# Performance work log

Hardware: AMD Instinct MI355X
Metric: run time of the kernel (lower is better)

## Reference

```python
import jax, jax.numpy as jnp
import numpy as np

NEG_BIG = -1e38

def setup_inputs() -> dict:
    key = jax.random.key(0)
    kq, kk, kv, kwq, kwk = jax.random.split(key, 5)
    B, S, d_model, d_k, d_v = 4, 4096, 256, 64, 64
    return {
        "q": jax.random.normal(kq, (B, S, d_model), dtype=jnp.float32),
        "k": jax.random.normal(kk, (B, S, d_model), dtype=jnp.float32),
        "v": jax.random.normal(kv, (B, S, d_v), dtype=jnp.float32),
        "w_q": jax.random.normal(kwq, (d_k, d_model), dtype=jnp.float32) * 0.01,
        "w_k": jax.random.normal(kwk, (d_k, d_model), dtype=jnp.float32) * 0.01,
    }

def reference(q, k, v, w_q, w_k):
    d_k = w_q.shape[0]
    temperature = jnp.asarray(np.power(d_k, 0.5), dtype=q.dtype)
    # relu-projected Q, K: [B,S,d_k]
    qp = jax.nn.relu(jnp.einsum("bsm,km->bsk", q, w_q))
    kp = jax.nn.relu(jnp.einsum("bsm,km->bsk", k, w_k))
    # scores [B,S,S]
    attn = jnp.einsum("bqd,bkd->bqk", qp, kp) / temperature
    # force column 0 to -1e38 (inline custom mask)
    attn = attn.at[:, :, 0].set(NEG_BIG)
    attn = jax.nn.softmax(attn, axis=2)
    # dropout is identity in eval / p=0
    out = jnp.einsum("bqk,bkd->bqd", attn, v)
    return out
```

## Files before the change

### kernel.cpp

```cpp
#include <hip/hip_runtime.h>

#define B_    4
#define S_    4096
#define DM    256
#define DK    64
#define NROWS (B_ * S_)
#define LOG2E 1.4426950408889634f
#define PACK_BIAS 0.0028151295f
#define NSPLIT 2
#define NJ     16

typedef __attribute__((ext_vector_type(8))) short bfrag;
typedef __attribute__((ext_vector_type(4))) float ffrag;

__device__ __forceinline__ unsigned bf16_rne_hi(float x) {
    unsigned u = __float_as_uint(x);
    return u + 0x7fffu + ((u >> 16) & 1u);
}
__device__ __forceinline__ unsigned short f2bf(float x) {
    return (unsigned short)(bf16_rne_hi(x) >> 16);
}
__device__ __forceinline__ unsigned pack_bf16x2(float lo, float hi) {
    return (bf16_rne_hi(hi) & 0xffff0000u) | (bf16_rne_hi(lo) >> 16);
}

__device__ __forceinline__ float fast_exp2(float x) {
#if __has_builtin(__builtin_amdgcn_exp2f)
    return __builtin_amdgcn_exp2f(x);
#else
    float r;
    asm("v_exp_f32 %0, %1\n\ts_nop 1" : "=v"(r) : "v"(x));
    return r;
#endif
}

__device__ __forceinline__ unsigned trunc_pack_bf16x2(float lo, float hi) {
    return __builtin_amdgcn_perm(__float_as_uint(hi), __float_as_uint(lo),
                                 0x07060302u);
}

__global__ __launch_bounds__(256) void fused_prep(
    const float* __restrict__ q, const float* __restrict__ k,
    const float* __restrict__ v, const float* __restrict__ wq,
    const float* __restrict__ wk, unsigned short* __restrict__ vT,
    unsigned short* __restrict__ qpb, unsigned short* __restrict__ kpb)
{
    __shared__ __align__(16) char smem[50688];
    const int blk  = blockIdx.x;
    const int lane = threadIdx.x & 63, w = threadIdx.x >> 6;

    if (blk < 256) {
        float (*tile)[65] = (float(*)[65])smem;
        const int b = blk >> 6, s0 = (blk & 63) * 64;
        const float4* src = (const float4*)(v + (size_t)(b * S_ + s0) * DK);
#pragma unroll
        for (int i = 0; i < 4; ++i) {
            const int idx4 = i * 256 + threadIdx.x;
            const int row = idx4 >> 4, c4 = idx4 & 15;
            const float4 vv = src[idx4];
            tile[row][c4 * 4 + 0] = vv.x;
            tile[row][c4 * 4 + 1] = vv.y;
            tile[row][c4 * 4 + 2] = vv.z;
            tile[row][c4 * 4 + 3] = vv.w;
        }
        __syncthreads();
        unsigned* dst = (unsigned*)(vT + (size_t)(b * 128 + (s0 >> 5)) * 64 * 32);
#pragma unroll
        for (int i = 0; i < 8; ++i) {
            const int u = i * 256 + threadIdx.x;
            const int t32 = u >> 10, rem = u & 1023;
            const int d = rem >> 4, c = rem & 15;
            dst[(t32 * 64 + d) * 16 + c] =
                pack_bf16x2(tile[t32 * 32 + c][d], tile[t32 * 32 + c + 16][d]);
        }
    } else {
        unsigned short* xlds = (unsigned short*)smem;
        unsigned short* wlds = (unsigned short*)(smem + 16896);
        const int pb = blk - 256;
        const int half = pb >> 9, rblk = pb & 511;
        const float* x;
        const float* wsrc;
        unsigned short* o;
        float scale;
        if (half == 0) { x = q; wsrc = wq; o = qpb; scale = 0.125f * LOG2E; }
        else           { x = k; wsrc = wk; o = kpb; scale = 1.0f; }

        const int rows0 = rblk * 32;
        const float4* xsrc = (const float4*)(x + (size_t)rows0 * DM);
#pragma unroll
        for (int i = 0; i < 8; ++i) {
            const int idx4 = i * 256 + threadIdx.x;
            const int row = idx4 >> 6, c4 = idx4 & 63;
            const float4 xv = xsrc[idx4];
            uint2 pk2;
            pk2.x = pack_bf16x2(xv.x, xv.y);
            pk2.y = pack_bf16x2(xv.z, xv.w);
            *(uint2*)&xlds[row * 264 + c4 * 4] = pk2;
        }
#pragma unroll
        for (int i = 0; i < 16; ++i) {
            const int idx4 = i * 256 + threadIdx.x;
            const int row = idx4 >> 6, c4 = idx4 & 63;
            const float4 wv = ((const float4*)wsrc)[idx4];
            uint2 pk2;
            pk2.x = pack_bf16x2(wv.x, wv.y);
            pk2.y = pack_bf16x2(wv.z, wv.w);
            *(uint2*)&wlds[row * 264 + c4 * 4] = pk2;
        }
        __syncthreads();

        const int m = lane & 15, quad = lane >> 4;

        ffrag acc[2];
        acc[0] = (ffrag)(0.0f);
        acc[1] = (ffrag)(0.0f);

#pragma unroll
        for (int kf = 0; kf < 8; ++kf) {
            const bfrag Bf = *(const bfrag*)&wlds[(w * 16 + m) * 264 + kf * 32 + quad * 8];
#pragma unroll
            for (int mt = 0; mt < 2; ++mt) {
                const bfrag A = *(const bfrag*)&xlds[(mt * 16 + m) * 264 + kf * 32 + quad * 8];
                acc[mt] = __builtin_amdgcn_mfma_f32_16x16x32_bf16(A, Bf, acc[mt], 0, 0, 0);
            }
        }
#pragma unroll
        for (int mt = 0; mt < 2; ++mt)
#pragma unroll
            for (int r = 0; r < 4; ++r)
                o[(rows0 + mt * 16 + quad * 4 + r) * DK + w * 16 + m] =
                    f2bf(fmaxf(acc[mt][r], 0.0f) * scale);
    }
}

__global__ __launch_bounds__(256) void attn_mfma(
    const unsigned short* __restrict__ qp, const unsigned short* __restrict__ kp,
    const unsigned short* __restrict__ vT, float* __restrict__ num_part,
    float* __restrict__ den_part)
{
    __shared__ __align__(16) char smem[20480];
    unsigned short* Plds = (unsigned short*)smem;
    float* red0 = (float*)smem;
    float* red1 = (float*)smem + 2560;

    const int lane = threadIdx.x & 63, w = threadIdx.x >> 6;
    const int m = lane & 15, quad = lane >> 4;
    const int sid = blockIdx.x & 7;
    const int b   = sid >> 1, gy = sid & 1;
    const int qgw = blockIdx.x >> 3;
    const int qbase = (b * 128 + qgw) * 32;
    const int kstart = (gy * 4 + w) * 512;

    bfrag qa[2][2];
#pragma unroll
    for (int mt = 0; mt < 2; ++mt)
#pragma unroll
        for (int kf = 0; kf < 2; ++kf)
            qa[mt][kf] = *(const bfrag*)&qp[(qbase + mt * 16 + m) * DK + kf * 32 + quad * 8];

    ffrag oacc[2][4];
    float dacc[2][4];
#pragma unroll
    for (int mt = 0; mt < 2; ++mt) {
#pragma unroll
        for (int dt = 0; dt < 4; ++dt) oacc[mt][dt] = (ffrag)(0.0f);
#pragma unroll
        for (int r = 0; r < 4; ++r) dacc[mt][r] = 0.0f;
    }

    const unsigned short* kptr = kp + ((size_t)b * S_ + kstart + m) * DK + quad * 8;
    const unsigned short* vptr = vT + ((size_t)(b * 128 + (kstart >> 5)) * 64 + m) * 32 + quad * 8;
    unsigned short* Pw = Plds + w * 1280;

    const ffrag cbias = (ffrag)(PACK_BIAS);

    bfrag kbuf[2][2][2], vbuf[2][4];
#pragma unroll
    for (int kt = 0; kt < 2; ++kt)
#pragma unroll
        for (int kf = 0; kf < 2; ++kf)
            kbuf[0][kt][kf] = *(const bfrag*)(kptr + kt * 1024 + kf * 32);
#pragma unroll
    for (int dt = 0; dt < 4; ++dt)
        vbuf[0][dt] = *(const bfrag*)(vptr + dt * 512);

    const unsigned short* knext = kptr + 2048;
    const unsigned short* vnext = vptr + 2048;

    bfrag pa0, pa1;

#pragma unroll 2
    for (int jj = 0; jj < NJ; ++jj) {
        const int p = jj & 1;

        if (jj < NJ - 1) {
#pragma unroll
            for (int kt = 0; kt < 2; ++kt)
#pragma unroll
                for (int kf = 0; kf < 2; ++kf)
                    kbuf[p ^ 1][kt][kf] = *(const bfrag*)(knext + kt * 1024 + kf * 32);
        }

        if (jj > 0) {
#pragma unroll
            for (int dt = 0; dt < 4; ++dt) {
                oacc[0][dt] = __builtin_amdgcn_mfma_f32_16x16x32_bf16(pa0, vbuf[p ^ 1][dt], oacc[0][dt], 0, 0, 0);
                oacc[1][dt] = __builtin_amdgcn_mfma_f32_16x16x32_bf16(pa1, vbuf[p ^ 1][dt], oacc[1][dt], 0, 0, 0);
            }
        }

        if (jj < NJ - 1) {
#pragma unroll
            for (int dt = 0; dt < 4; ++dt)
                vbuf[p ^ 1][dt] = *(const bfrag*)(vnext + dt * 512);
        }
        knext += 2048;
        vnext += 2048;

        ffrag s[2][2];
#pragma unroll
        for (int mt = 0; mt < 2; ++mt)
#pragma unroll
            for (int kt = 0; kt < 2; ++kt) {
                ffrag t = __builtin_amdgcn_mfma_f32_16x16x32_bf16(qa[mt][0], kbuf[p][kt][0], cbias, 0, 0, 0);
                s[mt][kt] = __builtin_amdgcn_mfma_f32_16x16x32_bf16(qa[mt][1], kbuf[p][kt][1], t, 0, 0, 0);
            }

        const bool mask0 = (jj == 0) && (kstart == 0) && (m == 0);
#pragma unroll
        for (int mt = 0; mt < 2; ++mt)
#pragma unroll
            for (int r = 0; r < 4; ++r) {
                float e0 = fast_exp2(s[mt][0][r]);
                float e1 = fast_exp2(s[mt][1][r]);
                if (mask0) e0 = 0.0f;
                dacc[mt][r] += e0 + e1;
                *(unsigned*)&Pw[(mt * 16 + quad * 4 + r) * 40 + m * 2] =
                    trunc_pack_bf16x2(e0, e1);
            }

        pa0 = *(const bfrag*)&Pw[(m) * 40 + quad * 8];
        pa1 = *(const bfrag*)&Pw[(16 + m) * 40 + quad * 8];
    }
#pragma unroll
    for (int dt = 0; dt < 4; ++dt) {
        oacc[0][dt] = __builtin_amdgcn_mfma_f32_16x16x32_bf16(pa0, vbuf[1][dt], oacc[0][dt], 0, 0, 0);
        oacc[1][dt] = __builtin_amdgcn_mfma_f32_16x16x32_bf16(pa1, vbuf[1][dt], oacc[1][dt], 0, 0, 0);
    }

#pragma unroll
    for (int mt = 0; mt < 2; ++mt)
#pragma unroll
        for (int r = 0; r < 4; ++r) {
            float d = dacc[mt][r];
            d += __shfl_xor(d, 1, 64);
            d += __shfl_xor(d, 2, 64);
            d += __shfl_xor(d, 4, 64);
            d += __shfl_xor(d, 8, 64);
            dacc[mt][r] = d;
        }

    __syncthreads();
    float* red[2] = { red0, red1 };
    if (w >= 2) {
#pragma unroll
        for (int mt = 0; mt < 2; ++mt) {
#pragma unroll
            for (int dt = 0; dt < 4; ++dt)
#pragma unroll
                for (int r = 0; r < 4; ++r)
                    red[w - 2][((mt * 4 + dt) * 4 + r) * 64 + lane] = oacc[mt][dt][r];
#pragma unroll
            for (int r = 0; r < 4; ++r)
                red[w - 2][2048 + (mt * 4 + r) * 64 + lane] = dacc[mt][r];
        }
    }
    __syncthreads();
    if (w < 2) {
#pragma unroll
        for (int mt = 0; mt < 2; ++mt) {
#pragma unroll
            for (int dt = 0; dt < 4; ++dt)
#pragma unroll
                for (int r = 0; r < 4; ++r)
                    oacc[mt][dt][r] += red[w][((mt * 4 + dt) * 4 + r) * 64 + lane];
#pragma unroll
            for (int r = 0; r < 4; ++r)
                dacc[mt][r] += red[w][2048 + (mt * 4 + r) * 64 + lane];
        }
    }
    __syncthreads();
    if (w == 1) {
#pragma unroll
        for (int mt = 0; mt < 2; ++mt) {
#pragma unroll
            for (int dt = 0; dt < 4; ++dt)
#pragma unroll
                for (int r = 0; r < 4; ++r)
                    red0[((mt * 4 + dt) * 4 + r) * 64 + lane] = oacc[mt][dt][r];
#pragma unroll
            for (int r = 0; r < 4; ++r)
                red0[2048 + (mt * 4 + r) * 64 + lane] = dacc[mt][r];
        }
    }
    __syncthreads();
    if (w == 0) {
#pragma unroll
        for (int mt = 0; mt < 2; ++mt) {
#pragma unroll
            for (int dt = 0; dt < 4; ++dt)
#pragma unroll
                for (int r = 0; r < 4; ++r) {
                    const float nv = oacc[mt][dt][r] + red0[((mt * 4 + dt) * 4 + r) * 64 + lane];
                    num_part[(size_t)gy * NROWS * DK +
                             (qbase + mt * 16 + quad * 4 + r) * DK + dt * 16 + m] = nv;
                }
#pragma unroll
            for (int r = 0; r < 4; ++r) {
                const float dv = dacc[mt][r] + red0[2048 + (mt * 4 + r) * 64 + lane];
                if (m == 0)
                    den_part[gy * NROWS + qbase + mt * 16 + quad * 4 + r] = dv;
            }
        }
    }
}

__global__ __launch_bounds__(256) void finalize_kernel(
    const float* __restrict__ num_part, const float* __restrict__ den_part,
    float* __restrict__ out)
{
    const int i4 = blockIdx.x * 256 + threadIdx.x;
    const int row = i4 >> 4;
    const float4 a = ((const float4*)num_part)[i4];
    const float4 c = ((const float4*)(num_part + (size_t)NROWS * DK))[i4];
    const float inv = 1.0f / (den_part[row] + den_part[NROWS + row]);
    float4 o;
    o.x = (a.x + c.x) * inv;
    o.y = (a.y + c.y) * inv;
    o.z = (a.z + c.z) * inv;
    o.w = (a.w + c.w) * inv;
    ((float4*)out)[i4] = o;
}

extern "C" void kernel_launch(void* const* d_in, const int* in_sizes, int n_in,
                              void* d_out, int out_size, void* d_ws, size_t ws_size,
                              hipStream_t stream)
{
    const float* q  = (const float*)d_in[0];
    const float* k  = (const float*)d_in[1];
    const float* v  = (const float*)d_in[2];
    const float* wq = (const float*)d_in[3];
    const float* wk = (const float*)d_in[4];
    float* out = (float*)d_out;

    char* p = (char*)d_ws;
    unsigned short* qpb = (unsigned short*)p;   p += (size_t)NROWS * DK * 2;
    unsigned short* kpb = (unsigned short*)p;   p += (size_t)NROWS * DK * 2;
    unsigned short* vT  = (unsigned short*)p;   p += (size_t)B_ * DK * S_ * 2;
    float* num_part     = (float*)p;            p += (size_t)NSPLIT * NROWS * DK * 4;
    float* den_part     = (float*)p;

    fused_prep<<<1280, 256, 0, stream>>>(q, k, v, wq, wk, vT, qpb, kpb);
    attn_mfma<<<1024, 256, 0, stream>>>(qpb, kpb, vT, num_part, den_part);
    finalize_kernel<<<NROWS * DK / 4 / 256, 256, 0, stream>>>(num_part, den_part, out);
}
```

Measured before the change: 139.5 us.

## Fuse prep, attention and finalize into one persistent kernel with grid barrier

Merges the three launches into a single 512-block kernel. Each block first does its share of the V transpose and Q/K projection, then waits on an atomic-counter grid barrier before running attention. The key split across blocks is removed, so each block now covers all keys with 4 waves of 1024 keys each and writes normalized output directly, dropping the partial numerator/denominator buffers and the finalize pass. The cost is a spin barrier that only works if all 512 blocks are resident at once, a memset launch to reset the counter, and half the grid parallelism in the attention phase with a longer per-wave loop.

Result: slower. 190.4 us (+36.5%).

```diff
diff --git a/kernel.cpp b/kernel.cpp
--- a/kernel.cpp
+++ b/kernel.cpp
@@ -7,8 +7,8 @@
 #define NROWS (B_ * S_)
 #define LOG2E 1.4426950408889634f
 #define PACK_BIAS 0.0028151295f
-#define NSPLIT 2
-#define NJ     16
+#define NJ 32
+#define GRID_BLKS 512
 
 typedef __attribute__((ext_vector_type(8))) short bfrag;
 typedef __attribute__((ext_vector_type(4))) float ffrag;
@@ -23,7 +23,6 @@
 __device__ __forceinline__ unsigned pack_bf16x2(float lo, float hi) {
     return (bf16_rne_hi(hi) & 0xffff0000u) | (bf16_rne_hi(lo) >> 16);
 }
-
 __device__ __forceinline__ float fast_exp2(float x) {
 #if __has_builtin(__builtin_amdgcn_exp2f)
     return __builtin_amdgcn_exp2f(x);
@@ -33,28 +32,29 @@
     return r;
 #endif
 }
-
 __device__ __forceinline__ unsigned trunc_pack_bf16x2(float lo, float hi) {
     return __builtin_amdgcn_perm(__float_as_uint(hi), __float_as_uint(lo),
                                  0x07060302u);
 }
 
-__global__ __launch_bounds__(256) void fused_prep(
+__global__ __launch_bounds__(256) void mega_kernel(
     const float* __restrict__ q, const float* __restrict__ k,
     const float* __restrict__ v, const float* __restrict__ wq,
-    const float* __restrict__ wk, unsigned short* __restrict__ vT,
-    unsigned short* __restrict__ qpb, unsigned short* __restrict__ kpb)
+    const float* __restrict__ wk, unsigned short* __restrict__ qpb,
+    unsigned short* __restrict__ kpb, unsigned short* __restrict__ vT,
+    unsigned* __restrict__ barrier_ctr, float* __restrict__ out)
 {
-    __shared__ __align__(16) char smem[50688];
-    const int blk  = blockIdx.x;
+    __shared__ __align__(16) char smem[20480];
     const int lane = threadIdx.x & 63, w = threadIdx.x >> 6;
-
-    if (blk < 256) {
+    const int m = lane & 15, quad = lane >> 4;
+    const int bp = blockIdx.x;
+
+    {
         float (*tile)[65] = (float(*)[65])smem;
-        const int b = blk >> 6, s0 = (blk & 63) * 64;
-        const float4* src = (const float4*)(v + (size_t)(b * S_ + s0) * DK);
-#pragma unroll
-        for (int i = 0; i < 4; ++i) {
+        const int b = bp >> 7, tt = bp & 127;
+        const float4* src = (const float4*)(v + ((size_t)b * S_ + tt * 32) * DK);
+#pragma unroll
+        for (int i = 0; i < 2; ++i) {
             const int idx4 = i * 256 + threadIdx.x;
             const int row = idx4 >> 4, c4 = idx4 & 15;
             const float4 vv = src[idx4];
@@ -64,99 +64,96 @@
             tile[row][c4 * 4 + 3] = vv.w;
         }
         __syncthreads();
-        unsigned* dst = (unsigned*)(vT + (size_t)(b * 128 + (s0 >> 5)) * 64 * 32);
-#pragma unroll
-        for (int i = 0; i < 8; ++i) {
+        unsigned* dst = (unsigned*)(vT + (size_t)bp * 2048);
+#pragma unroll
+        for (int i = 0; i < 4; ++i) {
             const int u = i * 256 + threadIdx.x;
-            const int t32 = u >> 10, rem = u & 1023;
-            const int d = rem >> 4, c = rem & 15;
-            dst[(t32 * 64 + d) * 16 + c] =
-                pack_bf16x2(tile[t32 * 32 + c][d], tile[t32 * 32 + c + 16][d]);
-        }
-    } else {
-        unsigned short* xlds = (unsigned short*)smem;
-        unsigned short* wlds = (unsigned short*)(smem + 16896);
-        const int pb = blk - 256;
-        const int half = pb >> 9, rblk = pb & 511;
-        const float* x;
-        const float* wsrc;
-        unsigned short* o;
-        float scale;
-        if (half == 0) { x = q; wsrc = wq; o = qpb; scale = 0.125f * LOG2E; }
-        else           { x = k; wsrc = wk; o = kpb; scale = 1.0f; }
-
-        const int rows0 = rblk * 32;
-        const float4* xsrc = (const float4*)(x + (size_t)rows0 * DM);
-#pragma unroll
-        for (int i = 0; i < 8; ++i) {
-            const int idx4 = i * 256 + threadIdx.x;
-            const int row = idx4 >> 6, c4 = idx4 & 63;
-            const float4 xv = xsrc[idx4];
-            uint2 pk2;
-            pk2.x = pack_bf16x2(xv.x, xv.y);
-            pk2.y = pack_bf16x2(xv.z, xv.w);
-            *(uint2*)&xlds[row * 264 + c4 * 4] = pk2;
-        }
-#pragma unroll
-        for (int i = 0; i < 16; ++i) {
-            const int idx4 = i * 256 + threadIdx.x;
-            const int row = idx4 >> 6, c4 = idx4 & 63;
-            const float4 wv = ((const float4*)wsrc)[idx4];
-            uint2 pk2;
-            pk2.x = pack_bf16x2(wv.x, wv.y);
-            pk2.y = pack_bf16x2(wv.z, wv.w);
-            *(uint2*)&wlds[row * 264 + c4 * 4] = pk2;
-        }
-        __syncthreads();
-
-        const int m = lane & 15, quad = lane >> 4;
-
-        ffrag acc[2];
-        acc[0] = (ffrag)(0.0f);
-        acc[1] = (ffrag)(0.0f);
-
+            const int d = u >> 4, c = u & 15;
+            dst[d * 16 + c] = pack_bf16x2(tile[c][d], tile[c + 16][d]);
+        }
+    }
+
+    {
+        const int half = bp >> 8, rblk = bp & 255;
+        const float* x = half ? k : q;
+        const float* wsrc = half ? wk : wq;
+        unsigned short* o = half ? kpb : qpb;
+        const float scale = half ? 1.0f : 0.125f * LOG2E;
+        const int rows0 = rblk * 64;
+
+        bfrag xa[8];
+        const float4* xrow = (const float4*)(x + (size_t)(rows0 + w * 16 + m) * DM);
 #pragma unroll
         for (int kf = 0; kf < 8; ++kf) {
-            const bfrag Bf = *(const bfrag*)&wlds[(w * 16 + m) * 264 + kf * 32 + quad * 8];
-#pragma unroll
-            for (int mt = 0; mt < 2; ++mt) {
-                const bfrag A = *(const bfrag*)&xlds[(mt * 16 + m) * 264 + kf * 32 + quad * 8];
-                acc[mt] = __builtin_amdgcn_mfma_f32_16x16x32_bf16(A, Bf, acc[mt], 0, 0, 0);
-            }
-        }
-#pragma unroll
-        for (int mt = 0; mt < 2; ++mt)
-#pragma unroll
-            for (int r = 0; r < 4; ++r)
-                o[(rows0 + mt * 16 + quad * 4 + r) * DK + w * 16 + m] =
-                    f2bf(fmaxf(acc[mt][r], 0.0f) * scale);
-    }
-}
-
-__global__ __launch_bounds__(256) void attn_mfma(
-    const unsigned short* __restrict__ qp, const unsigned short* __restrict__ kp,
-    const unsigned short* __restrict__ vT, float* __restrict__ num_part,
-    float* __restrict__ den_part)
-{
-    __shared__ __align__(16) char smem[20480];
+            const float4 a0 = xrow[kf * 8 + quad * 2];
+            const float4 a1 = xrow[kf * 8 + quad * 2 + 1];
+            union { bfrag v; unsigned u[4]; } pk;
+            pk.u[0] = pack_bf16x2(a0.x, a0.y);
+            pk.u[1] = pack_bf16x2(a0.z, a0.w);
+            pk.u[2] = pack_bf16x2(a1.x, a1.y);
+            pk.u[3] = pack_bf16x2(a1.z, a1.w);
+            xa[kf] = pk.v;
+        }
+
+        unsigned short* wlds = (unsigned short*)smem;
+#pragma unroll
+        for (int c = 0; c < 2; ++c) {
+            __syncthreads();
+            const float4* wsrc4 = (const float4*)(wsrc + c * 32 * DM);
+#pragma unroll
+            for (int i = 0; i < 8; ++i) {
+                const int idx4 = i * 256 + threadIdx.x;
+                const int row = idx4 >> 6, c4 = idx4 & 63;
+                const float4 wv = wsrc4[idx4];
+                uint2 pk2;
+                pk2.x = pack_bf16x2(wv.x, wv.y);
+                pk2.y = pack_bf16x2(wv.z, wv.w);
+                *(uint2*)&wlds[row * 264 + c4 * 4] = pk2;
+            }
+            __syncthreads();
+            ffrag a0 = (ffrag)(0.0f), a1 = (ffrag)(0.0f);
+#pragma unroll
+            for (int kf = 0; kf < 8; ++kf) {
+                const bfrag B0 = *(const bfrag*)&wlds[(m) * 264 + kf * 32 + quad * 8];
+                const bfrag B1 = *(const bfrag*)&wlds[(16 + m) * 264 + kf * 32 + quad * 8];
+                a0 = __builtin_amdgcn_mfma_f32_16x16x32_bf16(xa[kf], B0, a0, 0, 0, 0);
+                a1 = __builtin_amdgcn_mfma_f32_16x16x32_bf16(xa[kf], B1, a1, 0, 0, 0);
+            }
+#pragma unroll
+            for (int r = 0; r < 4; ++r) {
+                o[(rows0 + w * 16 + quad * 4 + r) * DK + c * 32 + m] =
+                    f2bf(fmaxf(a0[r], 0.0f) * scale);
+                o[(rows0 + w * 16 + quad * 4 + r) * DK + c * 32 + 16 + m] =
+                    f2bf(fmaxf(a1[r], 0.0f) * scale);
+            }
+        }
+    }
+
+    __syncthreads();
+    if (threadIdx.x == 0) {
+        __threadfence();
+        atomicAdd(barrier_ctr, 1u);
+        while (atomicAdd(barrier_ctr, 0u) < (unsigned)GRID_BLKS)
+            __builtin_amdgcn_s_sleep(8);
+        __threadfence();
+    }
+    __syncthreads();
+
     unsigned short* Plds = (unsigned short*)smem;
     float* red0 = (float*)smem;
     float* red1 = (float*)smem + 2560;
 
-    const int lane = threadIdx.x & 63, w = threadIdx.x >> 6;
-    const int m = lane & 15, quad = lane >> 4;
-    const int sid = blockIdx.x & 7;
-    const int b   = sid >> 1, gy = sid & 1;
-    const int qgw = blockIdx.x >> 3;
+    const int b   = bp & 3;
+    const int qgw = bp >> 2;
     const int qbase = (b * 128 + qgw) * 32;
-    const int kstart = (gy * 4 + w) * 512;
+    const int kstart = w * 1024;
 
     bfrag qa[2][2];
 #pragma unroll
     for (int mt = 0; mt < 2; ++mt)
 #pragma unroll
         for (int kf = 0; kf < 2; ++kf)
-            qa[mt][kf] = *(const bfrag*)&qp[(qbase + mt * 16 + m) * DK + kf * 32 + quad * 8];
+            qa[mt][kf] = *(const bfrag*)&qpb[(qbase + mt * 16 + m) * DK + kf * 32 + quad * 8];
 
     ffrag oacc[2][4];
     float dacc[2][4];
@@ -168,7 +165,7 @@
         for (int r = 0; r < 4; ++r) dacc[mt][r] = 0.0f;
     }
 
-    const unsigned short* kptr = kp + ((size_t)b * S_ + kstart + m) * DK + quad * 8;
+    const unsigned short* kptr = kpb + ((size_t)b * S_ + kstart + m) * DK + quad * 8;
     const unsigned short* vptr = vT + ((size_t)(b * 128 + (kstart >> 5)) * 64 + m) * 32 + quad * 8;
     unsigned short* Pw = Plds + w * 1280;
 
@@ -226,7 +223,7 @@
                 s[mt][kt] = __builtin_amdgcn_mfma_f32_16x16x32_bf16(qa[mt][1], kbuf[p][kt][1], t, 0, 0, 0);
             }
 
-        const bool mask0 = (jj == 0) && (kstart == 0) && (m == 0);
+        const bool mask0 = (jj == 0) && (w == 0) && (m == 0);
 #pragma unroll
         for (int mt = 0; mt < 2; ++mt)
 #pragma unroll
@@ -307,39 +304,19 @@
     if (w == 0) {
 #pragma unroll
         for (int mt = 0; mt < 2; ++mt) {
+            float inv[4];
+#pragma unroll
+            for (int r = 0; r < 4; ++r)
+                inv[r] = 1.0f / (dacc[mt][r] + red0[2048 + (mt * 4 + r) * 64 + lane]);
 #pragma unroll
             for (int dt = 0; dt < 4; ++dt)
 #pragma unroll
                 for (int r = 0; r < 4; ++r) {
                     const float nv = oacc[mt][dt][r] + red0[((mt * 4 + dt) * 4 + r) * 64 + lane];
-                    num_part[(size_t)gy * NROWS * DK +
-                             (qbase + mt * 16 + quad * 4 + r) * DK + dt * 16 + m] = nv;
+                    out[(qbase + mt * 16 + quad * 4 + r) * DK + dt * 16 + m] = nv * inv[r];
                 }
-#pragma unroll
-            for (int r = 0; r < 4; ++r) {
-                const float dv = dacc[mt][r] + red0[2048 + (mt * 4 + r) * 64 + lane];
-                if (m == 0)
-                    den_part[gy * NROWS + qbase + mt * 16 + quad * 4 + r] = dv;
-            }
-        }
-    }
-}
-
-__global__ __launch_bounds__(256) void finalize_kernel(
-    const float* __restrict__ num_part, const float* __restrict__ den_part,
-    float* __restrict__ out)
-{
-    const int i4 = blockIdx.x * 256 + threadIdx.x;
-    const int row = i4 >> 4;
-    const float4 a = ((const float4*)num_part)[i4];
-    const float4 c = ((const float4*)(num_part + (size_t)NROWS * DK))[i4];
-    const float inv = 1.0f / (den_part[row] + den_part[NROWS + row]);
-    float4 o;
-    o.x = (a.x + c.x) * inv;
-    o.y = (a.y + c.y) * inv;
-    o.z = (a.z + c.z) * inv;
-    o.w = (a.w + c.w) * inv;
-    ((float4*)out)[i4] = o;
+        }
+    }
 }
 
 extern "C" void kernel_launch(void* const* d_in, const int* in_sizes, int n_in,
@@ -357,10 +334,9 @@
     unsigned short* qpb = (unsigned short*)p;   p += (size_t)NROWS * DK * 2;
     unsigned short* kpb = (unsigned short*)p;   p += (size_t)NROWS * DK * 2;
     unsigned short* vT  = (unsigned short*)p;   p += (size_t)B_ * DK * S_ * 2;
-    float* num_part     = (float*)p;            p += (size_t)NSPLIT * NROWS * DK * 4;
-    float* den_part     = (float*)p;
-
-    fused_prep<<<1280, 256, 0, stream>>>(q, k, v, wq, wk, vT, qpb, kpb);
-    attn_mfma<<<1024, 256, 0, stream>>>(qpb, kpb, vT, num_part, den_part);
-    finalize_kernel<<<NROWS * DK / 4 / 256, 256, 0, stream>>>(num_part, den_part, out);
-}
+    unsigned* barrier_ctr = (unsigned*)p;
+
+    hipMemsetAsync(barrier_ctr, 0, 64, stream);
+    mega_kernel<<<GRID_BLKS, 256, 0, stream>>>(q, k, v, wq, wk, qpb, kpb, vT,
+                                               barrier_ctr, out);
+}
```

## Switch attention to 32x32x16 MFMA with register-resident P, removing LDS staging

Applied to the files above, without the earlier changes.

The attention kernel moves from 16x16x32 MFMAs to 32x32x16 MFMAs and computes S^T = K·Q^T, so each lane's exp outputs already sit in the B-operand layout for the P·V MFMA. This removes the per-iteration LDS write/read of P and the one-step software pipelining of the PV product. The V transpose in prep is permuted to match the new fragment layout. The numerator partials are now stored transposed per query group, so finalize stages them through LDS to transpose back, which adds shared-memory work there.

Measured after the change: 137.0 us. No clear change (-1.8%).

```diff
diff --git a/kernel.cpp b/kernel.cpp
--- a/kernel.cpp
+++ b/kernel.cpp
@@ -9,9 +9,11 @@
 #define PACK_BIAS 0.0028151295f
 #define NSPLIT 2
 #define NJ     16
-
-typedef __attribute__((ext_vector_type(8))) short bfrag;
-typedef __attribute__((ext_vector_type(4))) float ffrag;
+#define NQG    512
+
+typedef __attribute__((ext_vector_type(8)))  short bfrag;
+typedef __attribute__((ext_vector_type(4)))  float ffrag;
+typedef __attribute__((ext_vector_type(16))) float cfrag;
 
 __device__ __forceinline__ unsigned bf16_rne_hi(float x) {
     unsigned u = __float_as_uint(x);
@@ -23,7 +25,6 @@
 __device__ __forceinline__ unsigned pack_bf16x2(float lo, float hi) {
     return (bf16_rne_hi(hi) & 0xffff0000u) | (bf16_rne_hi(lo) >> 16);
 }
-
 __device__ __forceinline__ float fast_exp2(float x) {
 #if __has_builtin(__builtin_amdgcn_exp2f)
     return __builtin_amdgcn_exp2f(x);
@@ -33,7 +34,6 @@
     return r;
 #endif
 }
-
 __device__ __forceinline__ unsigned trunc_pack_bf16x2(float lo, float hi) {
     return __builtin_amdgcn_perm(__float_as_uint(hi), __float_as_uint(lo),
                                  0x07060302u);
@@ -70,8 +70,10 @@
             const int u = i * 256 + threadIdx.x;
             const int t32 = u >> 10, rem = u & 1023;
             const int d = rem >> 4, c = rem & 15;
+            const int C2 = (c & 1) | ((c & 2) << 1) | ((c & 4) >> 1) | (c & 8);
             dst[(t32 * 64 + d) * 16 + c] =
-                pack_bf16x2(tile[t32 * 32 + c][d], tile[t32 * 32 + c + 16][d]);
+                pack_bf16x2(tile[t32 * 32 + 2 * C2][d],
+                            tile[t32 * 32 + 2 * C2 + 1][d]);
         }
     } else {
         unsigned short* xlds = (unsigned short*)smem;
@@ -138,56 +140,46 @@
     const unsigned short* __restrict__ vT, float* __restrict__ num_part,
     float* __restrict__ den_part)
 {
-    __shared__ __align__(16) char smem[20480];
-    unsigned short* Plds = (unsigned short*)smem;
-    float* red0 = (float*)smem;
-    float* red1 = (float*)smem + 2560;
+    __shared__ float red[2][2112];
 
     const int lane = threadIdx.x & 63, w = threadIdx.x >> 6;
-    const int m = lane & 15, quad = lane >> 4;
+    const int l31 = lane & 31, g = lane >> 5;
     const int sid = blockIdx.x & 7;
     const int b   = sid >> 1, gy = sid & 1;
-    const int qgw = blockIdx.x >> 3;
-    const int qbase = (b * 128 + qgw) * 32;
+    const int qg  = blockIdx.x >> 3;
+    const int qgg = b * 128 + qg;
+    const int qbase = qgg * 32;
     const int kstart = (gy * 4 + w) * 512;
 
-    bfrag qa[2][2];
-#pragma unroll
-    for (int mt = 0; mt < 2; ++mt)
-#pragma unroll
-        for (int kf = 0; kf < 2; ++kf)
-            qa[mt][kf] = *(const bfrag*)&qp[(qbase + mt * 16 + m) * DK + kf * 32 + quad * 8];
-
-    ffrag oacc[2][4];
-    float dacc[2][4];
-#pragma unroll
-    for (int mt = 0; mt < 2; ++mt) {
-#pragma unroll
-        for (int dt = 0; dt < 4; ++dt) oacc[mt][dt] = (ffrag)(0.0f);
-#pragma unroll
-        for (int r = 0; r < 4; ++r) dacc[mt][r] = 0.0f;
-    }
-
-    const unsigned short* kptr = kp + ((size_t)b * S_ + kstart + m) * DK + quad * 8;
-    const unsigned short* vptr = vT + ((size_t)(b * 128 + (kstart >> 5)) * 64 + m) * 32 + quad * 8;
-    unsigned short* Pw = Plds + w * 1280;
-
-    const ffrag cbias = (ffrag)(PACK_BIAS);
-
-    bfrag kbuf[2][2][2], vbuf[2][4];
-#pragma unroll
-    for (int kt = 0; kt < 2; ++kt)
-#pragma unroll
-        for (int kf = 0; kf < 2; ++kf)
-            kbuf[0][kt][kf] = *(const bfrag*)(kptr + kt * 1024 + kf * 32);
-#pragma unroll
-    for (int dt = 0; dt < 4; ++dt)
-        vbuf[0][dt] = *(const bfrag*)(vptr + dt * 512);
+    bfrag qa[4];
+#pragma unroll
+    for (int s = 0; s < 4; ++s)
+        qa[s] = *(const bfrag*)&qp[(qbase + l31) * DK + s * 16 + g * 8];
+
+    cfrag oacc[2];
+    oacc[0] = (cfrag)(0.0f);
+    oacc[1] = (cfrag)(0.0f);
+    float dacc = 0.0f;
+
+    const unsigned short* kptr = kp + ((size_t)b * S_ + kstart + l31) * DK + g * 8;
+    const unsigned short* vptr = vT + ((size_t)(b * 128 + (kstart >> 5)) * 64 + l31) * 32 + g * 8;
+
+    cfrag cbias;
+#pragma unroll
+    for (int r = 0; r < 16; ++r) cbias[r] = PACK_BIAS;
+
+    bfrag kbuf[2][4], vbuf[2][2][2];
+#pragma unroll
+    for (int s = 0; s < 4; ++s)
+        kbuf[0][s] = *(const bfrag*)(kptr + s * 16);
+#pragma unroll
+    for (int h = 0; h < 2; ++h)
+#pragma unroll
+        for (int kc = 0; kc < 2; ++kc)
+            vbuf[0][h][kc] = *(const bfrag*)(vptr + h * 1024 + kc * 16);
 
     const unsigned short* knext = kptr + 2048;
     const unsigned short* vnext = vptr + 2048;
-
-    bfrag pa0, pa1;
 
 #pragma unroll 2
     for (int jj = 0; jj < NJ; ++jj) {
@@ -195,133 +187,91 @@
 
         if (jj < NJ - 1) {
 #pragma unroll
-            for (int kt = 0; kt < 2; ++kt)
-#pragma unroll
-                for (int kf = 0; kf < 2; ++kf)
-                    kbuf[p ^ 1][kt][kf] = *(const bfrag*)(knext + kt * 1024 + kf * 32);
-        }
-
-        if (jj > 0) {
-#pragma unroll
-            for (int dt = 0; dt < 4; ++dt) {
-                oacc[0][dt] = __builtin_amdgcn_mfma_f32_16x16x32_bf16(pa0, vbuf[p ^ 1][dt], oacc[0][dt], 0, 0, 0);
-                oacc[1][dt] = __builtin_amdgcn_mfma_f32_16x16x32_bf16(pa1, vbuf[p ^ 1][dt], oacc[1][dt], 0, 0, 0);
+            for (int s = 0; s < 4; ++s)
+                kbuf[p ^ 1][s] = *(const bfrag*)(knext + s * 16);
+#pragma unroll
+            for (int h = 0; h < 2; ++h)
+#pragma unroll
+                for (int kc = 0; kc < 2; ++kc)
+                    vbuf[p ^ 1][h][kc] = *(const bfrag*)(vnext + h * 1024 + kc * 16);
+            knext += 2048;
+            vnext += 2048;
+        }
+
+        cfrag c = cbias;
+#pragma unroll
+        for (int s = 0; s < 4; ++s)
+            c = __builtin_amdgcn_mfma_f32_32x32x16_bf16(kbuf[p][s], qa[s], c, 0, 0, 0);
+
+        float e[16];
+#pragma unroll
+        for (int r = 0; r < 16; ++r) e[r] = fast_exp2(c[r]);
+        if ((jj == 0) && (kstart == 0) && (g == 0)) e[0] = 0.0f;
+
+        dacc += (((e[0] + e[1]) + (e[2] + e[3])) + ((e[4] + e[5]) + (e[6] + e[7])))
+              + (((e[8] + e[9]) + (e[10] + e[11])) + ((e[12] + e[13]) + (e[14] + e[15])));
+
+        union { bfrag v; unsigned u[4]; } pf0, pf1;
+#pragma unroll
+        for (int d2 = 0; d2 < 4; ++d2) {
+            pf0.u[d2] = trunc_pack_bf16x2(e[2 * d2], e[2 * d2 + 1]);
+            pf1.u[d2] = trunc_pack_bf16x2(e[8 + 2 * d2], e[8 + 2 * d2 + 1]);
+        }
+
+#pragma unroll
+        for (int h = 0; h < 2; ++h) {
+            oacc[h] = __builtin_amdgcn_mfma_f32_32x32x16_bf16(vbuf[p][h][0], pf0.v, oacc[h], 0, 0, 0);
+            oacc[h] = __builtin_amdgcn_mfma_f32_32x32x16_bf16(vbuf[p][h][1], pf1.v, oacc[h], 0, 0, 0);
+        }
+    }
+
+    __syncthreads();
+    if (w >= 2) {
+#pragma unroll
+        for (int h = 0; h < 2; ++h)
+#pragma unroll
+            for (int r = 0; r < 16; ++r)
+                red[w - 2][(h * 16 + r) * 64 + lane] = oacc[h][r];
+        red[w - 2][2048 + lane] = dacc;
+    }
+    __syncthreads();
+    if (w < 2) {
+#pragma unroll
+        for (int h = 0; h < 2; ++h)
+#pragma unroll
+            for (int r = 0; r < 16; ++r)
+                oacc[h][r] += red[w][(h * 16 + r) * 64 + lane];
+        dacc += red[w][2048 + lane];
+    }
+    __syncthreads();
+    if (w == 1) {
+#pragma unroll
+        for (int h = 0; h < 2; ++h)
+#pragma unroll
+            for (int r = 0; r < 16; ++r)
+                red[0][(h * 16 + r) * 64 + lane] = oacc[h][r];
+        red[0][2048 + lane] = dacc;
+    }
+    __syncthreads();
+    if (w == 0) {
+#pragma unroll
+        for (int h = 0; h < 2; ++h)
+#pragma unroll
+            for (int r = 0; r < 16; ++r)
+                oacc[h][r] += red[0][(h * 16 + r) * 64 + lane];
+        dacc += red[0][2048 + lane];
+
+        float* np = num_part + ((size_t)gy * NQG + qgg) * 2048;
+#pragma unroll
+        for (int h = 0; h < 2; ++h)
+#pragma unroll
+            for (int r = 0; r < 16; ++r) {
+                const int d = h * 32 + (r & 3) + 8 * (r >> 2) + 4 * g;
+                np[d * 32 + l31] = oacc[h][r];
             }
-        }
-
-        if (jj < NJ - 1) {
-#pragma unroll
-            for (int dt = 0; dt < 4; ++dt)
-                vbuf[p ^ 1][dt] = *(const bfrag*)(vnext + dt * 512);
-        }
-        knext += 2048;
-        vnext += 2048;
-
-        ffrag s[2][2];
-#pragma unroll
-        for (int mt = 0; mt < 2; ++mt)
-#pragma unroll
-            for (int kt = 0; kt < 2; ++kt) {
-                ffrag t = __builtin_amdgcn_mfma_f32_16x16x32_bf16(qa[mt][0], kbuf[p][kt][0], cbias, 0, 0, 0);
-                s[mt][kt] = __builtin_amdgcn_mfma_f32_16x16x32_bf16(qa[mt][1], kbuf[p][kt][1], t, 0, 0, 0);
-            }
-
-        const bool mask0 = (jj == 0) && (kstart == 0) && (m == 0);
-#pragma unroll
-        for (int mt = 0; mt < 2; ++mt)
-#pragma unroll
-            for (int r = 0; r < 4; ++r) {
-                float e0 = fast_exp2(s[mt][0][r]);
-                float e1 = fast_exp2(s[mt][1][r]);
-                if (mask0) e0 = 0.0f;
-                dacc[mt][r] += e0 + e1;
-                *(unsigned*)&Pw[(mt * 16 + quad * 4 + r) * 40 + m * 2] =
-                    trunc_pack_bf16x2(e0, e1);
-            }
-
-        pa0 = *(const bfrag*)&Pw[(m) * 40 + quad * 8];
-        pa1 = *(const bfrag*)&Pw[(16 + m) * 40 + quad * 8];
-    }
-#pragma unroll
-    for (int dt = 0; dt < 4; ++dt) {
-        oacc[0][dt] = __builtin_amdgcn_mfma_f32_16x16x32_bf16(pa0, vbuf[1][dt], oacc[0][dt], 0, 0, 0);
-        oacc[1][dt] = __builtin_amdgcn_mfma_f32_16x16x32_bf16(pa1, vbuf[1][dt], oacc[1][dt], 0, 0, 0);
-    }
-
-#pragma unroll
-    for (int mt = 0; mt < 2; ++mt)
-#pragma unroll
-        for (int r = 0; r < 4; ++r) {
-            float d = dacc[mt][r];
-            d += __shfl_xor(d, 1, 64);
-            d += __shfl_xor(d, 2, 64);
-            d += __shfl_xor(d, 4, 64);
-            d += __shfl_xor(d, 8, 64);
-            dacc[mt][r] = d;
-        }
-
-    __syncthreads();
-    float* red[2] = { red0, red1 };
-    if (w >= 2) {
-#pragma unroll
-        for (int mt = 0; mt < 2; ++mt) {
-#pragma unroll
-            for (int dt = 0; dt < 4; ++dt)
-#pragma unroll
-                for (int r = 0; r < 4; ++r)
-                    red[w - 2][((mt * 4 + dt) * 4 + r) * 64 + lane] = oacc[mt][dt][r];
-#pragma unroll
-            for (int r = 0; r < 4; ++r)
-                red[w - 2][2048 + (mt * 4 + r) * 64 + lane] = dacc[mt][r];
-        }
-    }
-    __syncthreads();
-    if (w < 2) {
-#pragma unroll
-        for (int mt = 0; mt < 2; ++mt) {
-#pragma unroll
-            for (int dt = 0; dt < 4; ++dt)
-#pragma unroll
-                for (int r = 0; r < 4; ++r)
-                    oacc[mt][dt][r] += red[w][((mt * 4 + dt) * 4 + r) * 64 + lane];
-#pragma unroll
-            for (int r = 0; r < 4; ++r)
-                dacc[mt][r] += red[w][2048 + (mt * 4 + r) * 64 + lane];
-        }
-    }
-    __syncthreads();
-    if (w == 1) {
-#pragma unroll
-        for (int mt = 0; mt < 2; ++mt) {
-#pragma unroll
-            for (int dt = 0; dt < 4; ++dt)
-#pragma unroll
-                for (int r = 0; r < 4; ++r)
-                    red0[((mt * 4 + dt) * 4 + r) * 64 + lane] = oacc[mt][dt][r];
-#pragma unroll
-            for (int r = 0; r < 4; ++r)
-                red0[2048 + (mt * 4 + r) * 64 + lane] = dacc[mt][r];
-        }
-    }
-    __syncthreads();
-    if (w == 0) {
-#pragma unroll
-        for (int mt = 0; mt < 2; ++mt) {
-#pragma unroll
-            for (int dt = 0; dt < 4; ++dt)
-#pragma unroll
-                for (int r = 0; r < 4; ++r) {
-                    const float nv = oacc[mt][dt][r] + red0[((mt * 4 + dt) * 4 + r) * 64 + lane];
-                    num_part[(size_t)gy * NROWS * DK +
-                             (qbase + mt * 16 + quad * 4 + r) * DK + dt * 16 + m] = nv;
-                }
-#pragma unroll
-            for (int r = 0; r < 4; ++r) {
-                const float dv = dacc[mt][r] + red0[2048 + (mt * 4 + r) * 64 + lane];
-                if (m == 0)
-                    den_part[gy * NROWS + qbase + mt * 16 + quad * 4 + r] = dv;
-            }
-        }
+        const float dtot = dacc + __shfl_xor(dacc, 32, 64);
+        if (g == 0)
+            den_part[gy * NROWS + qbase + l31] = dtot;
     }
 }
 
@@ -329,17 +279,30 @@
     const float* __restrict__ num_part, const float* __restrict__ den_part,
     float* __restrict__ out)
 {
-    const int i4 = blockIdx.x * 256 + threadIdx.x;
-    const int row = i4 >> 4;
-    const float4 a = ((const float4*)num_part)[i4];
-    const float4 c = ((const float4*)(num_part + (size_t)NROWS * DK))[i4];
-    const float inv = 1.0f / (den_part[row] + den_part[NROWS + row]);
-    float4 o;
-    o.x = (a.x + c.x) * inv;
-    o.y = (a.y + c.y) * inv;
-    o.z = (a.z + c.z) * inv;
-    o.w = (a.w + c.w) * inv;
-    ((float4*)out)[i4] = o;
+    __shared__ float trans[64][33];
+    __shared__ float invd[32];
+    const int qg = blockIdx.x;
+    const int t  = threadIdx.x;
+
+    if (t < 32)
+        invd[t] = 1.0f / (den_part[qg * 32 + t] + den_part[NROWS + qg * 32 + t]);
+    __syncthreads();
+
+    const float* np0 = num_part + (size_t)qg * 2048;
+    const float* np1 = num_part + (size_t)NQG * 2048 + (size_t)qg * 2048;
+#pragma unroll
+    for (int i = 0; i < 8; ++i) {
+        const int idx = i * 256 + t;
+        const int d = idx >> 5, qq = idx & 31;
+        trans[d][qq] = (np0[idx] + np1[idx]) * invd[qq];
+    }
+    __syncthreads();
+    float* ob = out + (size_t)qg * 2048;
+#pragma unroll
+    for (int i = 0; i < 8; ++i) {
+        const int j = i * 256 + t;
+        ob[j] = trans[j & 63][j >> 6];
+    }
 }
 
 extern "C" void kernel_launch(void* const* d_in, const int* in_sizes, int n_in,
@@ -362,5 +325,5 @@
 
     fused_prep<<<1280, 256, 0, stream>>>(q, k, v, wq, wk, vT, qpb, kpb);
     attn_mfma<<<1024, 256, 0, stream>>>(qpb, kpb, vT, num_part, den_part);
-    finalize_kernel<<<NROWS * DK / 4 / 256, 256, 0, stream>>>(num_part, den_part, out);
-}
+    finalize_kernel<<<NQG, 256, 0, stream>>>(num_part, den_part, out);
+}
```
